# Performance work log

Measured on AMD Instinct MI355X. Metric: run time of the kernel, lower is better.

Reference implementation:

```python
import jax, jax.numpy as jnp
import numpy as np

KWTA = 16          # number of winners (kwta)
THRESH = 16384.0   # firing threshold


def setup_inputs() -> dict:
    key = jax.random.key(0)
    k1, k2 = jax.random.split(key)
    # SpykeTorch layout: (timesteps, in_channels, H, W)
    rec_field = jax.random.uniform(k1, (64, 1, 256, 256), dtype=jnp.float32)
    # LocalConvolution weight: kernel covers the full receptive field -> (k, C, kh, kw)
    weight = jax.random.uniform(k2, (2048, 1, 256, 256), dtype=jnp.float32)
    return {"rec_field": rec_field, "weight": weight}


def reference(rec_field, weight):
    T = rec_field.shape[0]
    K = weight.shape[0]
    # LocalConvolution with kernel == receptive field: output spatial dims are 1x1,
    # i.e. a dense projection of the flattened field onto K cells -> (T, K)
    out = jnp.einsum('tchw,kchw->tk', rec_field, weight)
    # sf.fire(out, thresh, True): threshold_ keeps values strictly > thresh, else 0
    pot = jnp.where(out > THRESH, out, jnp.zeros((), out.dtype))  # thresholded potentials
    spikes = jnp.sign(pot)                                        # 0/1 spike wave
    # sf.get_k_winners(pot, kwta, inhibition_radius=0); spikes = pot.sign()
    n_spk = spikes.sum(axis=0)                                    # (K,)
    # index of earliest spike timestep per feature, clamped to [0, T-1]
    first_idx = jnp.clip((T - n_spk).astype(jnp.int32), 0, T - 1)
    first_pot = jnp.take_along_axis(pot, first_idx[None, :], axis=0)  # (1, K)
    trunc = spikes * first_pot                                    # (T, K)
    v = trunc.max() * T                                           # large bias at spike positions
    total = (trunc + spikes * v).sum(axis=0)                      # (K,) ranking score
    # iterative argmax + zeroing of the winning feature (radius 0) == top-k,
    # with the loop's break-on-zero handled by the validity mask
    top_vals, top_idx = jax.lax.top_k(total, KWTA)
    valid = (top_vals > 0).astype(out.dtype)
    coef = jnp.zeros((K,), dtype=out.dtype).at[top_idx].set(valid)  # winner channel mask
    # coef broadcast over timesteps; restore (T, K, 1, 1) spatial layout
    return jnp.sign(pot * coef[None, :])[:, :, None, None]
```

## Files before the change

### kernel.cpp

```cpp
#include <hip/hip_runtime.h>


typedef int i32x4 __attribute__((ext_vector_type(4)));

constexpr int KDIM   = 65536;
constexpr int NCOL   = 2048;
constexpr int TROWS  = 64;
constexpr int SPLIT  = 16;
constexpr int KRANGE = KDIM / SPLIT;
constexpr int KS     = 64;
constexpr int STAGES = KRANGE / KS;
constexpr int LROWB  = 80;
constexpr int PSTB   = TROWS * LROWB;
constexpr long long THRESH_I = 1LL << 60;
constexpr unsigned long long C_OFF = 8421504ull;
constexpr unsigned long long C2T   = 65536ull * C_OFF * C_OFF;

__device__ __forceinline__ void cvt4(const float4 f, unsigned& p0, unsigned& p1,
                                     unsigned& p2, unsigned& s4) {
    const unsigned k0 = (unsigned)(f.x * 8388608.0f);
    const unsigned k1 = (unsigned)(f.y * 8388608.0f);
    const unsigned k2 = (unsigned)(f.z * 8388608.0f);
    const unsigned k3 = (unsigned)(f.w * 8388608.0f);
    s4 = k0 + k1 + k2 + k3;
    unsigned a01, a23;
    a01 = __builtin_amdgcn_perm(k1, k0, 0x0c0c0400u);
    a23 = __builtin_amdgcn_perm(k3, k2, 0x0c0c0400u);
    p0  = __builtin_amdgcn_perm(a23, a01, 0x05040100u) ^ 0x80808080u;
    a01 = __builtin_amdgcn_perm(k1, k0, 0x0c0c0501u);
    a23 = __builtin_amdgcn_perm(k3, k2, 0x0c0c0501u);
    p1  = __builtin_amdgcn_perm(a23, a01, 0x05040100u) ^ 0x80808080u;
    a01 = __builtin_amdgcn_perm(k1, k0, 0x0c0c0602u);
    a23 = __builtin_amdgcn_perm(k3, k2, 0x0c0c0602u);
    p2  = __builtin_amdgcn_perm(a23, a01, 0x05040100u) ^ 0x80808080u;
}

__global__ __launch_bounds__(256, 2) void gemm_i8(const float* __restrict__ A,
                                                  const float* __restrict__ W,
                                                  unsigned long long* __restrict__ P,
                                                  unsigned long long* __restrict__ Ra,
                                                  unsigned long long* __restrict__ Sw) {
    __shared__ char Al[3 * PSTB];
    __shared__ char Wl[3 * PSTB];
    const int tid  = threadIdx.x;
    const int lane = tid & 63;
    const int wv   = tid >> 6;
    const int r0   = (wv >> 1) * 32;
    const int c0   = (wv & 1) * 32;
    const int colBase = blockIdx.x * 64;
    const int kBase   = blockIdx.y * KRANGE;

    const int lrow = tid >> 2;
    const int cch  = (tid & 3) * 16;

    const int frow = lane & 15;
    const int fkB  = (lane >> 4) * 16;

    i32x4 acc[5][2][2] = {};
    unsigned long long sumA = 0, sumW = 0;

    for (int st = 0; st < STAGES; ++st) {
        const int k0 = kBase + st * KS;
        float4 av[4], wv4[4];
        const float* ap = A + (size_t)lrow * KDIM + k0 + cch;
        const float* wp = W + (size_t)(colBase + lrow) * KDIM + k0 + cch;
#pragma unroll
        for (int i = 0; i < 4; ++i) av[i] = ((const float4*)ap)[i];
#pragma unroll
        for (int i = 0; i < 4; ++i) wv4[i] = ((const float4*)wp)[i];

        unsigned pa[3][4], pw[3][4], sA = 0, sW = 0, s4;
#pragma unroll
        for (int g = 0; g < 4; ++g) { cvt4(av[g],  pa[0][g], pa[1][g], pa[2][g], s4); sA += s4; }
#pragma unroll
        for (int g = 0; g < 4; ++g) { cvt4(wv4[g], pw[0][g], pw[1][g], pw[2][g], s4); sW += s4; }
        sumA += sA; sumW += sW;

        __syncthreads();
#pragma unroll
        for (int p = 0; p < 3; ++p) {
            *(i32x4*)(Al + p * PSTB + lrow * LROWB + cch) =
                (i32x4){(int)pa[p][0], (int)pa[p][1], (int)pa[p][2], (int)pa[p][3]};
            *(i32x4*)(Wl + p * PSTB + lrow * LROWB + cch) =
                (i32x4){(int)pw[p][0], (int)pw[p][1], (int)pw[p][2], (int)pw[p][3]};
        }
        __syncthreads();

        i32x4 af[3][2], bf[3][2];
#pragma unroll
        for (int p = 0; p < 3; ++p)
#pragma unroll
            for (int rt = 0; rt < 2; ++rt)
                af[p][rt] = *(const i32x4*)(Al + p * PSTB + (r0 + rt * 16 + frow) * LROWB + fkB);
#pragma unroll
        for (int p = 0; p < 3; ++p)
#pragma unroll
            for (int ct = 0; ct < 2; ++ct)
                bf[p][ct] = *(const i32x4*)(Wl + p * PSTB + (c0 + ct * 16 + frow) * LROWB + fkB);

#pragma unroll
        for (int p = 0; p < 3; ++p)
#pragma unroll
            for (int q = 0; q < 3; ++q) {
                const int s = p + q;
#pragma unroll
                for (int rt = 0; rt < 2; ++rt)
#pragma unroll
                    for (int ct = 0; ct < 2; ++ct)
                        acc[s][rt][ct] = __builtin_amdgcn_mfma_i32_16x16x64_i8(
                            af[p][rt], bf[q][ct], acc[s][rt][ct], 0, 0, 0);
            }
    }

#pragma unroll
    for (int rt = 0; rt < 2; ++rt)
#pragma unroll
        for (int ct = 0; ct < 2; ++ct)
#pragma unroll
            for (int r = 0; r < 4; ++r) {
                long long t = 0;
#pragma unroll
                for (int s = 0; s < 5; ++s)
                    t += ((long long)acc[s][rt][ct][r]) << (8 * s);
                const int row = r0 + rt * 16 + (lane >> 4) * 4 + r;
                const int col = colBase + c0 + ct * 16 + (lane & 15);
                atomicAdd(&P[(size_t)row * NCOL + col], (unsigned long long)t);
            }

    sumA += __shfl_down(sumA, 2); sumA += __shfl_down(sumA, 1);
    sumW += __shfl_down(sumW, 2); sumW += __shfl_down(sumW, 1);
    if ((tid & 3) == 0) {
        atomicAdd(&Sw[colBase + lrow], sumW);
        if (blockIdx.x == 0) atomicAdd(&Ra[lrow], sumA);
    }
}

__global__ __launch_bounds__(256) void colstats(const unsigned long long* __restrict__ P,
                                                const unsigned long long* __restrict__ Ra,
                                                const unsigned long long* __restrict__ Sw,
                                                int* __restrict__ nspk,
                                                long long* __restrict__ fpot,
                                                unsigned long long* __restrict__ mbits) {
    const int k = blockIdx.x * blockDim.x + threadIdx.x;
    const unsigned long long swk = Sw[k];
    int n = 0;
    for (int t = 0; t < TROWS; ++t) {
        const long long v = (long long)(P[(size_t)t * NCOL + k] + C_OFF * (Ra[t] + swk) - C2T);
        n += (v > THRESH_I) ? 1 : 0;
    }
    int fi = TROWS - n;
    if (fi > TROWS - 1) fi = TROWS - 1;
    const long long c  = (long long)(P[(size_t)fi * NCOL + k] + C_OFF * (Ra[fi] + swk) - C2T);
    const long long fp = (c > THRESH_I) ? c : 0;
    nspk[k] = n;
    fpot[k] = fp;
    atomicMax(mbits, (unsigned long long)fp);
}

__global__ __launch_bounds__(256) void topk16(const long long* __restrict__ fpot,
                                              const int* __restrict__ nspk,
                                              const unsigned long long* __restrict__ mbits,
                                              unsigned int* __restrict__ coef) {
    __shared__ long long sf[NCOL];
    __shared__ int sn[NCOL];
    __shared__ long long rv[256];
    __shared__ int rn[256];
    __shared__ int ri[256];
    const int tid = threadIdx.x;
    const bool anyv = (*mbits) > 0ull;
    for (int k = tid; k < NCOL; k += 256) { sf[k] = fpot[k]; sn[k] = nspk[k]; }
    __syncthreads();

    for (int round = 0; round < 16; ++round) {
        int bn = -1; long long bf = -1; int bi = 1 << 30;
        for (int k = tid; k < NCOL; k += 256) {
            const int nn = sn[k]; const long long ff = sf[k];
            if (nn > bn || (nn == bn && (ff > bf || (ff == bf && k < bi)))) {
                bn = nn; bf = ff; bi = k;
            }
        }
        rn[tid] = bn; rv[tid] = bf; ri[tid] = bi;
        __syncthreads();
        for (int s = 128; s > 0; s >>= 1) {
            if (tid < s) {
                const int on = rn[tid + s]; const long long of = rv[tid + s]; const int oi = ri[tid + s];
                if (on > rn[tid] || (on == rn[tid] && (of > rv[tid] || (of == rv[tid] && oi < ri[tid])))) {
                    rn[tid] = on; rv[tid] = of; ri[tid] = oi;
                }
            }
            __syncthreads();
        }
        if (tid == 0) {
            const int w = ri[0];
            if (rn[0] > 0 && anyv) coef[w] = 1u;
            sn[w] = -1;
        }
        __syncthreads();
    }
}

__global__ __launch_bounds__(256) void writeout(const unsigned long long* __restrict__ P,
                                                const unsigned long long* __restrict__ Ra,
                                                const unsigned long long* __restrict__ Sw,
                                                const unsigned int* __restrict__ coef,
                                                float* __restrict__ out) {
    const int idx = blockIdx.x * blockDim.x + threadIdx.x;
    const int t = idx >> 11;
    const int k = idx & (NCOL - 1);
    const long long v = (long long)(P[idx] + C_OFF * (Ra[t] + Sw[k]) - C2T);
    out[idx] = (coef[k] != 0u && v > THRESH_I) ? 1.0f : 0.0f;
}

extern "C" void kernel_launch(void* const* d_in, const int* in_sizes, int n_in,
                              void* d_out, int out_size, void* d_ws, size_t ws_size,
                              hipStream_t stream) {
    (void)in_sizes; (void)n_in; (void)out_size; (void)ws_size;
    const float* A = (const float*)d_in[0];
    const float* W = (const float*)d_in[1];
    float* out = (float*)d_out;

    char* ws = (char*)d_ws;
    unsigned long long* P     = (unsigned long long*)ws;
    unsigned long long* mbits = (unsigned long long*)(ws + 1048576);
    unsigned int*       coef  = (unsigned int*)(ws + 1048576 + 8);
    unsigned long long* Ra    = (unsigned long long*)(ws + 1048576 + 8 + 8192);
    unsigned long long* Sw    = (unsigned long long*)(ws + 1048576 + 8 + 8192 + 512);
    long long* fpot = (long long*)(ws + 1048576 + 8 + 8192 + 512 + 16384);
    int*       nspk = (int*)(ws + 1048576 + 8 + 8192 + 512 + 16384 + 16384);
    const size_t zero_bytes = 1048576 + 8 + 8192 + 512 + 16384;

    hipMemsetAsync(d_ws, 0, zero_bytes, stream);

    gemm_i8<<<dim3(NCOL / 64, SPLIT), 256, 0, stream>>>(A, W, P, Ra, Sw);
    colstats<<<NCOL / 256, 256, 0, stream>>>(P, Ra, Sw, nspk, fpot, mbits);
    topk16<<<1, 256, 0, stream>>>(fpot, nspk, mbits, coef);
    writeout<<<(TROWS * NCOL) / 256, 256, 0, stream>>>(P, Ra, Sw, coef, out);
}
```

Baseline: 784.0 us.

## Double-buffer LDS in int8 GEMM and reuse spike bitmask in writeout

The GEMM main loop now double-buffers the shared-memory tiles. It prefetches the next stage's global loads before the MFMA work and converts and stages them into the other buffer afterward, so each stage needs one barrier instead of two. This aims to hide global load latency behind tensor-core work. Separately, colstats records a per-column 64-bit spike mask, which writeout uses instead of rereading P and recomputing the potentials. The cost is double the LDS footprint and more live registers, which may pressure occupancy under the 2-blocks-per-CU launch bound.

```diff
diff --git a/kernel.cpp b/kernel.cpp
--- a/kernel.cpp
+++ b/kernel.cpp
@@ -35,13 +35,47 @@
     p2  = __builtin_amdgcn_perm(a23, a01, 0x05040100u) ^ 0x80808080u;
 }
 
+__device__ __forceinline__ void loadAW(const float* __restrict__ A, const float* __restrict__ W,
+                                       int lrow, int cch, int colBase, int k0,
+                                       float4 (&av)[4], float4 (&wv)[4]) {
+    const float* ap = A + (size_t)lrow * KDIM + k0 + cch;
+    const float* wp = W + (size_t)(colBase + lrow) * KDIM + k0 + cch;
+#pragma unroll
+    for (int i = 0; i < 4; ++i) av[i] = ((const float4*)ap)[i];
+#pragma unroll
+    for (int i = 0; i < 4; ++i) wv[i] = ((const float4*)wp)[i];
+}
+
+__device__ __forceinline__ void cvtAW(const float4 (&av)[4], const float4 (&wv)[4],
+                                      unsigned (&pa)[3][4], unsigned (&pw)[3][4],
+                                      unsigned long long& sumA, unsigned long long& sumW) {
+    unsigned sA = 0, sW = 0, s4;
+#pragma unroll
+    for (int g = 0; g < 4; ++g) { cvt4(av[g], pa[0][g], pa[1][g], pa[2][g], s4); sA += s4; }
+#pragma unroll
+    for (int g = 0; g < 4; ++g) { cvt4(wv[g], pw[0][g], pw[1][g], pw[2][g], s4); sW += s4; }
+    sumA += sA; sumW += sW;
+}
+
+__device__ __forceinline__ void stageAW(char* __restrict__ Al, char* __restrict__ Wl,
+                                        int lrow, int cch,
+                                        const unsigned (&pa)[3][4], const unsigned (&pw)[3][4]) {
+#pragma unroll
+    for (int p = 0; p < 3; ++p) {
+        *(i32x4*)(Al + p * PSTB + lrow * LROWB + cch) =
+            (i32x4){(int)pa[p][0], (int)pa[p][1], (int)pa[p][2], (int)pa[p][3]};
+        *(i32x4*)(Wl + p * PSTB + lrow * LROWB + cch) =
+            (i32x4){(int)pw[p][0], (int)pw[p][1], (int)pw[p][2], (int)pw[p][3]};
+    }
+}
+
 __global__ __launch_bounds__(256, 2) void gemm_i8(const float* __restrict__ A,
                                                   const float* __restrict__ W,
                                                   unsigned long long* __restrict__ P,
                                                   unsigned long long* __restrict__ Ra,
                                                   unsigned long long* __restrict__ Sw) {
-    __shared__ char Al[3 * PSTB];
-    __shared__ char Wl[3 * PSTB];
+    __shared__ char Al[2][3 * PSTB];
+    __shared__ char Wl[2][3 * PSTB];
     const int tid  = threadIdx.x;
     const int lane = tid & 63;
     const int wv   = tid >> 6;
@@ -59,44 +93,30 @@
     i32x4 acc[5][2][2] = {};
     unsigned long long sumA = 0, sumW = 0;
 
+    float4 av[4], wv4[4];
+    unsigned pa[3][4], pw[3][4];
+
+    loadAW(A, W, lrow, cch, colBase, kBase, av, wv4);
+    cvtAW(av, wv4, pa, pw, sumA, sumW);
+    stageAW(Al[0], Wl[0], lrow, cch, pa, pw);
+    __syncthreads();
+
     for (int st = 0; st < STAGES; ++st) {
-        const int k0 = kBase + st * KS;
-        float4 av[4], wv4[4];
-        const float* ap = A + (size_t)lrow * KDIM + k0 + cch;
-        const float* wp = W + (size_t)(colBase + lrow) * KDIM + k0 + cch;
-#pragma unroll
-        for (int i = 0; i < 4; ++i) av[i] = ((const float4*)ap)[i];
-#pragma unroll
-        for (int i = 0; i < 4; ++i) wv4[i] = ((const float4*)wp)[i];
-
-        unsigned pa[3][4], pw[3][4], sA = 0, sW = 0, s4;
-#pragma unroll
-        for (int g = 0; g < 4; ++g) { cvt4(av[g],  pa[0][g], pa[1][g], pa[2][g], s4); sA += s4; }
-#pragma unroll
-        for (int g = 0; g < 4; ++g) { cvt4(wv4[g], pw[0][g], pw[1][g], pw[2][g], s4); sW += s4; }
-        sumA += sA; sumW += sW;
-
-        __syncthreads();
-#pragma unroll
-        for (int p = 0; p < 3; ++p) {
-            *(i32x4*)(Al + p * PSTB + lrow * LROWB + cch) =
-                (i32x4){(int)pa[p][0], (int)pa[p][1], (int)pa[p][2], (int)pa[p][3]};
-            *(i32x4*)(Wl + p * PSTB + lrow * LROWB + cch) =
-                (i32x4){(int)pw[p][0], (int)pw[p][1], (int)pw[p][2], (int)pw[p][3]};
-        }
-        __syncthreads();
+        const int cur = st & 1;
+        if (st + 1 < STAGES)
+            loadAW(A, W, lrow, cch, colBase, kBase + (st + 1) * KS, av, wv4);
 
         i32x4 af[3][2], bf[3][2];
 #pragma unroll
         for (int p = 0; p < 3; ++p)
 #pragma unroll
             for (int rt = 0; rt < 2; ++rt)
-                af[p][rt] = *(const i32x4*)(Al + p * PSTB + (r0 + rt * 16 + frow) * LROWB + fkB);
+                af[p][rt] = *(const i32x4*)(Al[cur] + p * PSTB + (r0 + rt * 16 + frow) * LROWB + fkB);
 #pragma unroll
         for (int p = 0; p < 3; ++p)
 #pragma unroll
             for (int ct = 0; ct < 2; ++ct)
-                bf[p][ct] = *(const i32x4*)(Wl + p * PSTB + (c0 + ct * 16 + frow) * LROWB + fkB);
+                bf[p][ct] = *(const i32x4*)(Wl[cur] + p * PSTB + (c0 + ct * 16 + frow) * LROWB + fkB);
 
 #pragma unroll
         for (int p = 0; p < 3; ++p)
@@ -110,6 +130,12 @@
                         acc[s][rt][ct] = __builtin_amdgcn_mfma_i32_16x16x64_i8(
                             af[p][rt], bf[q][ct], acc[s][rt][ct], 0, 0, 0);
             }
+
+        if (st + 1 < STAGES) {
+            cvtAW(av, wv4, pa, pw, sumA, sumW);
+            stageAW(Al[cur ^ 1], Wl[cur ^ 1], lrow, cch, pa, pw);
+        }
+        __syncthreads();
     }
 
 #pragma unroll
@@ -140,13 +166,15 @@
                                                 const unsigned long long* __restrict__ Sw,
                                                 int* __restrict__ nspk,
                                                 long long* __restrict__ fpot,
-                                                unsigned long long* __restrict__ mbits) {
+                                                unsigned long long* __restrict__ mbits,
+                                                unsigned long long* __restrict__ smask) {
     const int k = blockIdx.x * blockDim.x + threadIdx.x;
     const unsigned long long swk = Sw[k];
     int n = 0;
+    unsigned long long mask = 0;
     for (int t = 0; t < TROWS; ++t) {
         const long long v = (long long)(P[(size_t)t * NCOL + k] + C_OFF * (Ra[t] + swk) - C2T);
-        n += (v > THRESH_I) ? 1 : 0;
+        if (v > THRESH_I) { ++n; mask |= (1ull << t); }
     }
     int fi = TROWS - n;
     if (fi > TROWS - 1) fi = TROWS - 1;
@@ -154,6 +182,7 @@
     const long long fp = (c > THRESH_I) ? c : 0;
     nspk[k] = n;
     fpot[k] = fp;
+    smask[k] = mask;
     atomicMax(mbits, (unsigned long long)fp);
 }
 
@@ -199,16 +228,13 @@
     }
 }
 
-__global__ __launch_bounds__(256) void writeout(const unsigned long long* __restrict__ P,
-                                                const unsigned long long* __restrict__ Ra,
-                                                const unsigned long long* __restrict__ Sw,
+__global__ __launch_bounds__(256) void writeout(const unsigned long long* __restrict__ smask,
                                                 const unsigned int* __restrict__ coef,
                                                 float* __restrict__ out) {
     const int idx = blockIdx.x * blockDim.x + threadIdx.x;
     const int t = idx >> 11;
     const int k = idx & (NCOL - 1);
-    const long long v = (long long)(P[idx] + C_OFF * (Ra[t] + Sw[k]) - C2T);
-    out[idx] = (coef[k] != 0u && v > THRESH_I) ? 1.0f : 0.0f;
+    out[idx] = (coef[k] != 0u && ((smask[k] >> t) & 1ull)) ? 1.0f : 0.0f;
 }
 
 extern "C" void kernel_launch(void* const* d_in, const int* in_sizes, int n_in,
@@ -227,12 +253,13 @@
     unsigned long long* Sw    = (unsigned long long*)(ws + 1048576 + 8 + 8192 + 512);
     long long* fpot = (long long*)(ws + 1048576 + 8 + 8192 + 512 + 16384);
     int*       nspk = (int*)(ws + 1048576 + 8 + 8192 + 512 + 16384 + 16384);
+    unsigned long long* smask = (unsigned long long*)(ws + 1048576 + 8 + 8192 + 512 + 16384 + 16384 + 8192);
     const size_t zero_bytes = 1048576 + 8 + 8192 + 512 + 16384;
 
     hipMemsetAsync(d_ws, 0, zero_bytes, stream);
 
     gemm_i8<<<dim3(NCOL / 64, SPLIT), 256, 0, stream>>>(A, W, P, Ra, Sw);
-    colstats<<<NCOL / 256, 256, 0, stream>>>(P, Ra, Sw, nspk, fpot, mbits);
+    colstats<<<NCOL / 256, 256, 0, stream>>>(P, Ra, Sw, nspk, fpot, mbits, smask);
     topk16<<<1, 256, 0, stream>>>(fpot, nspk, mbits, coef);
-    writeout<<<(TROWS * NCOL) / 256, 256, 0, stream>>>(P, Ra, Sw, coef, out);
-}
+    writeout<<<(TROWS * NCOL) / 256, 256, 0, stream>>>(smask, coef, out);
+}
```

Measured after the change: 838.4 us. 1.07x slower.
